# Performance work log

Hardware: AMD Instinct MI355X
Metric: run time of the kernel (lower is better)

The kernel has to match this reference:

```python
import jax, jax.numpy as jnp
import numpy as np

LAMBDA_BOX = 1.0
LAMBDA_OBJ = 1.0
IOU_THRESHOLD = 0.2
ALPHA = 0.25
GAMMA = 2.0
EPS = 1e-7  # torchvision complete_box_iou_loss eps


def box_cxcywh_to_xyxy(boxes):
    # boxes [..., 4] (cx, cy, w, h); w,h clamped to min 1e-4 as in the torch code
    cx, cy, w, h = jnp.split(boxes, 4, axis=-1)
    w = jnp.maximum(w, 1e-4)
    h = jnp.maximum(h, 1e-4)
    return jnp.concatenate([cx - w / 2, cy - h / 2, cx + w / 2, cy + h / 2], axis=-1)


def pairwise_box_iou(a, b):
    # a [B,N,4] xyxy, b [B,M,4] xyxy -> [B,N,M] (torchvision box_iou: inter/union, no eps)
    a = a[:, :, None, :]  # [B,N,1,4]
    b = b[:, None, :, :]  # [B,1,M,4]
    lt = jnp.maximum(a[..., :2], b[..., :2])
    rb = jnp.minimum(a[..., 2:], b[..., 2:])
    wh = jnp.clip(rb - lt, 0.0)
    inter = wh[..., 0] * wh[..., 1]
    area_a = (a[..., 2] - a[..., 0]) * (a[..., 3] - a[..., 1])
    area_b = (b[..., 2] - b[..., 0]) * (b[..., 3] - b[..., 1])
    return inter / (area_a + area_b - inter)


def ciou_loss(p, t):
    # torchvision.ops.complete_box_iou_loss, elementwise over [...,4] xyxy boxes
    x1p, y1p, x2p, y2p = p[..., 0], p[..., 1], p[..., 2], p[..., 3]
    x1t, y1t, x2t, y2t = t[..., 0], t[..., 1], t[..., 2], t[..., 3]
    lt_x = jnp.maximum(x1p, x1t); lt_y = jnp.maximum(y1p, y1t)
    rb_x = jnp.minimum(x2p, x2t); rb_y = jnp.minimum(y2p, y2t)
    inter = jnp.clip(rb_x - lt_x, 0.0) * jnp.clip(rb_y - lt_y, 0.0)
    union = (x2p - x1p) * (y2p - y1p) + (x2t - x1t) * (y2t - y1t) - inter
    iou = inter / (union + EPS)
    # smallest enclosing box diagonal
    cx1 = jnp.minimum(x1p, x1t); cy1 = jnp.minimum(y1p, y1t)
    cx2 = jnp.maximum(x2p, x2t); cy2 = jnp.maximum(y2p, y2t)
    diag = (cx2 - cx1) ** 2 + (cy2 - cy1) ** 2 + EPS
    centers = ((x1p + x2p - x1t - x2t) ** 2 + (y1p + y2p - y1t - y2t) ** 2) / 4.0
    diou = 1.0 - iou + centers / diag
    wp = x2p - x1p; hp = y2p - y1p
    wt = x2t - x1t; ht = y2t - y1t
    v = (4.0 / (jnp.pi ** 2)) * (jnp.arctan(wt / ht) - jnp.arctan(wp / hp)) ** 2
    alpha = jax.lax.stop_gradient(v / (1.0 - iou + v + EPS))
    return diou + alpha * v


def focal_loss_mean(logits, targets):
    # mean over last axis; matches torch focal_loss with alpha=0.25, gamma=2
    prob = jax.nn.sigmoid(logits)
    # stable BCE-with-logits
    ce = jnp.clip(logits, 0.0) - logits * targets + jnp.log1p(jnp.exp(-jnp.abs(logits)))
    p_t = prob * targets + (1.0 - prob) * (1.0 - targets)
    alpha_t = ALPHA * targets + (1.0 - ALPHA) * (1.0 - targets)
    p_t = jnp.clip(p_t, 1e-6, 1.0 - 1e-6)
    return (alpha_t * (1.0 - p_t) ** GAMMA * ce).mean(axis=-1)


def greedy_match(iou_nm):
    # iou_nm [N,M]: sequential greedy per-GT matching with conf_target gating
    N = iou_nm.shape[0]
    def step(conf_t, iou_col):
        best = jnp.argmax(iou_col)
        ok = (iou_col[best] > IOU_THRESHOLD) & (conf_t[best] < 0.01)
        conf_t = jnp.where(ok, conf_t.at[best].set(1.0), conf_t)
        return conf_t, (best, ok)
    conf_target, (idx, mask) = jax.lax.scan(step, jnp.zeros((N,), iou_nm.dtype), iou_nm.T)
    return conf_target, idx, mask


def setup_inputs() -> dict:
    key = jax.random.key(0)
    k1, k2, k3, k4, k5 = jax.random.split(key, 5)
    B, N, M = 16, 25000, 64
    # predictions: cx,cy in [0,1], w,h in [0.02,0.3], conf logit ~ N(0,1)
    pcxy = jax.random.uniform(k1, (B, N, 2), jnp.float32)
    pwh = jax.random.uniform(k2, (B, N, 2), jnp.float32, 0.02, 0.3)
    pconf = jax.random.normal(k3, (B, N, 1), jnp.float32)
    preds = jnp.concatenate([pcxy, pwh, pconf], axis=-1)
    # GT boxes in xyxy (as consumed directly by box_iou in the torch code)
    gcxy = jax.random.uniform(k4, (B, M, 2), jnp.float32)
    gwh = jax.random.uniform(k5, (B, M, 2), jnp.float32, 0.02, 0.3)
    targets = box_cxcywh_to_xyxy(jnp.concatenate([gcxy, gwh], axis=-1))
    return {"preds": preds, "targets": targets}


def reference(preds, targets):
    # preds [B,N,5], targets [B,M,4] xyxy -> scalar loss
    pred_xyxy = box_cxcywh_to_xyxy(preds[..., :4])  # [B,N,4]
    pred_conf = preds[..., 4]                        # [B,N]
    # matching indices are non-differentiable (argmax selection)
    iou_m = pairwise_box_iou(jax.lax.stop_gradient(pred_xyxy),
                             jax.lax.stop_gradient(targets))  # [B,N,M]
    conf_target, idx, mask = jax.vmap(greedy_match)(iou_m)  # [B,N], [B,M], [B,M]
    conf_loss = focal_loss_mean(pred_conf, conf_target)      # [B]
    # gather matched pred boxes and compute masked-mean CIoU loss per image
    pb = jnp.take_along_axis(pred_xyxy, idx[..., None], axis=1)  # [B,M,4]
    ciou = ciou_loss(pb, targets)                                # [B,M]
    m = mask.astype(ciou.dtype)
    n_match = m.sum(axis=1)
    box_loss = (ciou * m).sum(axis=1) / jnp.maximum(n_match, 1.0)
    per_image = LAMBDA_OBJ * conf_loss + jnp.where(n_match > 0, LAMBDA_BOX * box_loss, 0.0)
    return per_image.mean()
```

## Files before the change

kernel.cpp:

```cpp
#include <hip/hip_runtime.h>
#include <math.h>

#define BATCH 16
#define NPRED 25000
#define MTGT  64
#define CHUNKS 32
#define PPC   800
#define ABLK  512
#define WAVES (ABLK / 64)
#define PPW   (PPC / WAVES)

#define GMAX_OFF 256
#define WS_ZERO_BYTES (GMAX_OFF + BATCH * MTGT * 8)

__device__ __forceinline__ float focal_term(float x, float t) {
    float prob = 1.0f / (1.0f + expf(-x));
    float ce = fmaxf(x, 0.0f) - x * t + log1pf(expf(-fabsf(x)));
    float p_t = prob * t + (1.0f - prob) * (1.0f - t);
    float alpha_t = 0.25f * t + 0.75f * (1.0f - t);
    p_t = fminf(fmaxf(p_t, 1e-6f), 1.0f - 1e-6f);
    float om = 1.0f - p_t;
    return alpha_t * om * om * ce;
}

__global__ __launch_bounds__(ABLK) void iou_argmax_kernel(
    const float* __restrict__ preds,
    const float* __restrict__ targets,
    unsigned long long* __restrict__ gmax,
    float* __restrict__ focal0)
{
    const int b = blockIdx.y;
    const int chunk = blockIdx.x;
    const int t = threadIdx.x;
    const int lane = t & 63;
    const int w = t >> 6;

    __shared__ float4 sbox[PPC];
    __shared__ unsigned long long comb[WAVES][MTGT];
    __shared__ float sfocal[WAVES];

    float fsum = 0.0f;
    for (int idx = t; idx < PPC; idx += ABLK) {
        int n = chunk * PPC + idx;
        float4 bx;
        if (n < NPRED) {
            const float* p = preds + ((long)b * NPRED + n) * 5;
            float cx = p[0], cy = p[1];
            float wd = fmaxf(p[2], 1e-4f);
            float hh = fmaxf(p[3], 1e-4f);
            bx.x = cx - wd / 2.0f;
            bx.y = cy - hh / 2.0f;
            bx.z = cx + wd / 2.0f;
            bx.w = cy + hh / 2.0f;
            fsum += focal_term(p[4], 0.0f);
        } else {
            bx = make_float4(3e8f, 3e8f, 3e8f, 3e8f);
        }
        sbox[idx] = bx;
    }
    for (int off = 32; off > 0; off >>= 1) fsum += __shfl_down(fsum, off);
    if (lane == 0) sfocal[w] = fsum;

    const float* tg = targets + ((long)b * MTGT + lane) * 4;
    float tx1 = tg[0], ty1 = tg[1], tx2 = tg[2], ty2 = tg[3];
    float ta = (tx2 - tx1) * (ty2 - ty1);

    __syncthreads();

    const int nbase = chunk * PPC + w * PPW;
    float best_i = 0.0f, best_d = 1.0f;
    int best_n = nbase;
#pragma unroll 4
    for (int j = 0; j < PPW; j++) {
        float4 bx = sbox[w * PPW + j];
        float ap = (bx.z - bx.x) * (bx.w - bx.y);
        float ltx = fmaxf(bx.x, tx1), lty = fmaxf(bx.y, ty1);
        float rbx = fminf(bx.z, tx2), rby = fminf(bx.w, ty2);
        float inter = fmaxf(rbx - ltx, 0.0f) * fmaxf(rby - lty, 0.0f);
        float den = ap + ta - inter;
        bool better = (inter * best_d) > (best_i * den);
        best_i = better ? inter : best_i;
        best_d = better ? den : best_d;
        best_n = better ? (nbase + j) : best_n;
    }
    float iou = best_i / best_d;
    comb[w][lane] =
        ((unsigned long long)__float_as_uint(iou) << 32) | (unsigned int)(~best_n);

    __syncthreads();

    if (t < MTGT) {
        unsigned long long v = comb[0][t];
        for (int ww = 1; ww < WAVES; ww++) {
            unsigned long long o = comb[ww][t];
            v = (o > v) ? o : v;
        }
        atomicMax(&gmax[b * MTGT + t], v);
    }
    if (t == 0) {
        float s = 0.0f;
        for (int ww = 0; ww < WAVES; ww++) s += sfocal[ww];
        atomicAdd(&focal0[b], s);
    }
}

__global__ __launch_bounds__(64) void finalize_kernel(
    const float* __restrict__ preds,
    const float* __restrict__ targets,
    const unsigned long long* __restrict__ gmax,
    const float* __restrict__ focal0,
    float* __restrict__ out)
{
    const int b = blockIdx.x;
    const int t = threadIdx.x;

    unsigned long long packed = gmax[b * MTGT + t];
    int id = (int)(~(unsigned int)packed);

    const float* tgp = targets + ((long)b * MTGT + t) * 4;
    float x1t = tgp[0], y1t = tgp[1], x2t = tgp[2], y2t = tgp[3];

    float x1p = 0.f, y1p = 0.f, x2p = 0.f, y2p = 0.f, cf = 0.f;
    float v = 0.0f;
    if (id >= 0 && id < NPRED) {
        const float* p = preds + ((long)b * NPRED + id) * 5;
        float cx = p[0], cy = p[1];
        float wd = fmaxf(p[2], 1e-4f);
        float hh = fmaxf(p[3], 1e-4f);
        cf = p[4];
        x1p = cx - wd / 2.0f; y1p = cy - hh / 2.0f;
        x2p = cx + wd / 2.0f; y2p = cy + hh / 2.0f;
        float ltx = fmaxf(x1p, x1t), lty = fmaxf(y1p, y1t);
        float rbx = fminf(x2p, x2t), rby = fminf(y2p, y2t);
        float inter = fmaxf(rbx - ltx, 0.0f) * fmaxf(rby - lty, 0.0f);
        float ap = (x2p - x1p) * (y2p - y1p);
        float at = (x2t - x1t) * (y2t - y1t);
        v = inter / (ap + at - inter);
    }

    bool accepted = false;
    for (int m = 0; m < MTGT; m++) {
        float vm = __shfl(v, m);
        int im = __shfl(id, m);
        unsigned long long conflict = __ballot(accepted && (id == im));
        bool ok = (vm > 0.2f) && (conflict == 0ull);
        if (t == m) accepted = ok;
    }

    float csum = 0.0f, dsum = 0.0f;
    int cnt = 0;
    if (accepted) {
        float ltx = fmaxf(x1p, x1t), lty = fmaxf(y1p, y1t);
        float rbx = fminf(x2p, x2t), rby = fminf(y2p, y2t);
        float inter = fmaxf(rbx - ltx, 0.0f) * fmaxf(rby - lty, 0.0f);
        float uni = (x2p - x1p) * (y2p - y1p) + (x2t - x1t) * (y2t - y1t) - inter;
        float iou = inter / (uni + 1e-7f);
        float cx1 = fminf(x1p, x1t), cy1 = fminf(y1p, y1t);
        float cx2 = fmaxf(x2p, x2t), cy2 = fmaxf(y2p, y2t);
        float dx = cx2 - cx1, dy = cy2 - cy1;
        float diag = dx * dx + dy * dy + 1e-7f;
        float ex = x1p + x2p - x1t - x2t;
        float ey = y1p + y2p - y1t - y2t;
        float centers = (ex * ex + ey * ey) / 4.0f;
        float diou = 1.0f - iou + centers / diag;
        float wp = x2p - x1p, hp = y2p - y1p;
        float wt = x2t - x1t, ht = y2t - y1t;
        float dat = atanf(wt / ht) - atanf(wp / hp);
        float vv = 0.40528473f * (dat * dat);
        float alpha = vv / (1.0f - iou + vv + 1e-7f);
        csum = diou + alpha * vv;
        cnt = 1;
        dsum = focal_term(cf, 1.0f) - focal_term(cf, 0.0f);
    }

    for (int off = 32; off > 0; off >>= 1) {
        csum += __shfl_down(csum, off);
        dsum += __shfl_down(dsum, off);
        cnt  += __shfl_down(cnt, off);
    }
    if (t == 0) {
        float conf = (focal0[b] + dsum) / (float)NPRED;
        float per = conf;
        if (cnt > 0) per += csum / (float)cnt;
        atomicAdd(out, per * (1.0f / (float)BATCH));
    }
}

extern "C" void kernel_launch(void* const* d_in, const int* in_sizes, int n_in,
                              void* d_out, int out_size, void* d_ws, size_t ws_size,
                              hipStream_t stream) {
    const float* preds = (const float*)d_in[0];
    const float* targets = (const float*)d_in[1];
    float* out = (float*)d_out;

    float* focal0 = (float*)d_ws;
    unsigned long long* gmax = (unsigned long long*)((char*)d_ws + GMAX_OFF);

    hipMemsetAsync(d_out, 0, sizeof(float), stream);
    hipMemsetAsync(d_ws, 0, WS_ZERO_BYTES, stream);

    dim3 gridA(CHUNKS, BATCH);
    iou_argmax_kernel<<<gridA, ABLK, 0, stream>>>(preds, targets, gmax, focal0);
    finalize_kernel<<<BATCH, 64, 0, stream>>>(preds, targets, gmax, focal0, out);
}
```

Baseline: 87.54 us.

## Replace global atomics and memsets with per-chunk partials reduced in single-block finalize

```diff
diff --git a/kernel.cpp b/kernel.cpp
--- a/kernel.cpp
+++ b/kernel.cpp
@@ -10,8 +10,8 @@
 #define WAVES (ABLK / 64)
 #define PPW   (PPC / WAVES)
 
-#define GMAX_OFF 256
-#define WS_ZERO_BYTES (GMAX_OFF + BATCH * MTGT * 8)
+#define CAND_OFF 0
+#define FOCALP_OFF (BATCH * CHUNKS * MTGT * 8)
 
 __device__ __forceinline__ float focal_term(float x, float t) {
     float prob = 1.0f / (1.0f + expf(-x));
@@ -26,8 +26,8 @@
 __global__ __launch_bounds__(ABLK) void iou_argmax_kernel(
     const float* __restrict__ preds,
     const float* __restrict__ targets,
-    unsigned long long* __restrict__ gmax,
-    float* __restrict__ focal0)
+    unsigned long long* __restrict__ cand,
+    float* __restrict__ focalp)
 {
     const int b = blockIdx.y;
     const int chunk = blockIdx.x;
@@ -36,6 +36,7 @@
     const int w = t >> 6;
 
     __shared__ float4 sbox[PPC];
+    __shared__ float sarea[PPC];
     __shared__ unsigned long long comb[WAVES][MTGT];
     __shared__ float sfocal[WAVES];
 
@@ -57,6 +58,7 @@
             bx = make_float4(3e8f, 3e8f, 3e8f, 3e8f);
         }
         sbox[idx] = bx;
+        sarea[idx] = (bx.z - bx.x) * (bx.w - bx.y);
     }
     for (int off = 32; off > 0; off >>= 1) fsum += __shfl_down(fsum, off);
     if (lane == 0) sfocal[w] = fsum;
@@ -67,13 +69,12 @@
 
     __syncthreads();
 
-    const int nbase = chunk * PPC + w * PPW;
     float best_i = 0.0f, best_d = 1.0f;
-    int best_n = nbase;
+    int best_j = 0;
 #pragma unroll 4
     for (int j = 0; j < PPW; j++) {
         float4 bx = sbox[w * PPW + j];
-        float ap = (bx.z - bx.x) * (bx.w - bx.y);
+        float ap = sarea[w * PPW + j];
         float ltx = fmaxf(bx.x, tx1), lty = fmaxf(bx.y, ty1);
         float rbx = fminf(bx.z, tx2), rby = fminf(bx.w, ty2);
         float inter = fmaxf(rbx - ltx, 0.0f) * fmaxf(rby - lty, 0.0f);
@@ -81,8 +82,9 @@
         bool better = (inter * best_d) > (best_i * den);
         best_i = better ? inter : best_i;
         best_d = better ? den : best_d;
-        best_n = better ? (nbase + j) : best_n;
-    }
+        best_j = better ? j : best_j;
+    }
+    int best_n = chunk * PPC + w * PPW + best_j;
     float iou = best_i / best_d;
     comb[w][lane] =
         ((unsigned long long)__float_as_uint(iou) << 32) | (unsigned int)(~best_n);
@@ -95,29 +97,38 @@
             unsigned long long o = comb[ww][t];
             v = (o > v) ? o : v;
         }
-        atomicMax(&gmax[b * MTGT + t], v);
+        cand[((long)b * CHUNKS + chunk) * MTGT + t] = v;
     }
     if (t == 0) {
         float s = 0.0f;
         for (int ww = 0; ww < WAVES; ww++) s += sfocal[ww];
-        atomicAdd(&focal0[b], s);
-    }
-}
-
-__global__ __launch_bounds__(64) void finalize_kernel(
+        focalp[b * CHUNKS + chunk] = s;
+    }
+}
+
+__global__ __launch_bounds__(BATCH * 64) void finalize_kernel(
     const float* __restrict__ preds,
     const float* __restrict__ targets,
-    const unsigned long long* __restrict__ gmax,
-    const float* __restrict__ focal0,
+    const unsigned long long* __restrict__ cand,
+    const float* __restrict__ focalp,
     float* __restrict__ out)
 {
-    const int b = blockIdx.x;
     const int t = threadIdx.x;
-
-    unsigned long long packed = gmax[b * MTGT + t];
+    const int b = t >> 6;
+    const int lane = t & 63;
+
+    __shared__ float sper[BATCH];
+
+    const unsigned long long* cb = cand + ((long)b * CHUNKS) * MTGT + lane;
+    unsigned long long packed = cb[0];
+#pragma unroll
+    for (int c = 1; c < CHUNKS; c++) {
+        unsigned long long o = cb[(long)c * MTGT];
+        packed = (o > packed) ? o : packed;
+    }
     int id = (int)(~(unsigned int)packed);
 
-    const float* tgp = targets + ((long)b * MTGT + t) * 4;
+    const float* tgp = targets + ((long)b * MTGT + lane) * 4;
     float x1t = tgp[0], y1t = tgp[1], x2t = tgp[2], y2t = tgp[3];
 
     float x1p = 0.f, y1p = 0.f, x2p = 0.f, y2p = 0.f, cf = 0.f;
@@ -144,11 +155,12 @@
         int im = __shfl(id, m);
         unsigned long long conflict = __ballot(accepted && (id == im));
         bool ok = (vm > 0.2f) && (conflict == 0ull);
-        if (t == m) accepted = ok;
-    }
-
-    float csum = 0.0f, dsum = 0.0f;
+        if (lane == m) accepted = ok;
+    }
+
+    float csum = 0.0f;
     int cnt = 0;
+    float dsum = (lane < CHUNKS) ? focalp[b * CHUNKS + lane] : 0.0f;
     if (accepted) {
         float ltx = fmaxf(x1p, x1t), lty = fmaxf(y1p, y1t);
         float rbx = fminf(x2p, x2t), rby = fminf(y2p, y2t);
@@ -170,7 +182,7 @@
         float alpha = vv / (1.0f - iou + vv + 1e-7f);
         csum = diou + alpha * vv;
         cnt = 1;
-        dsum = focal_term(cf, 1.0f) - focal_term(cf, 0.0f);
+        dsum += focal_term(cf, 1.0f) - focal_term(cf, 0.0f);
     }
 
     for (int off = 32; off > 0; off >>= 1) {
@@ -178,11 +190,16 @@
         dsum += __shfl_down(dsum, off);
         cnt  += __shfl_down(cnt, off);
     }
+    if (lane == 0) {
+        float per = dsum / (float)NPRED;
+        if (cnt > 0) per += csum / (float)cnt;
+        sper[b] = per;
+    }
+    __syncthreads();
     if (t == 0) {
-        float conf = (focal0[b] + dsum) / (float)NPRED;
-        float per = conf;
-        if (cnt > 0) per += csum / (float)cnt;
-        atomicAdd(out, per * (1.0f / (float)BATCH));
+        float s = 0.0f;
+        for (int i = 0; i < BATCH; i++) s += sper[i];
+        out[0] = s / (float)BATCH;
     }
 }
 
@@ -193,13 +210,10 @@
     const float* targets = (const float*)d_in[1];
     float* out = (float*)d_out;
 
-    float* focal0 = (float*)d_ws;
-    unsigned long long* gmax = (unsigned long long*)((char*)d_ws + GMAX_OFF);
-
-    hipMemsetAsync(d_out, 0, sizeof(float), stream);
-    hipMemsetAsync(d_ws, 0, WS_ZERO_BYTES, stream);
+    unsigned long long* cand = (unsigned long long*)((char*)d_ws + CAND_OFF);
+    float* focalp = (float*)((char*)d_ws + FOCALP_OFF);
 
     dim3 gridA(CHUNKS, BATCH);
-    iou_argmax_kernel<<<gridA, ABLK, 0, stream>>>(preds, targets, gmax, focal0);
-    finalize_kernel<<<BATCH, 64, 0, stream>>>(preds, targets, gmax, focal0, out);
-}
+    iou_argmax_kernel<<<gridA, ABLK, 0, stream>>>(preds, targets, cand, focalp);
+    finalize_kernel<<<1, BATCH * 64, 0, stream>>>(preds, targets, cand, focalp, out);
+}
```

Measured after the change: 86.02 us. About the same (-1.7%).
